# Optimization experiments

Hardware: AMD Instinct MI355X
Metric: run time of the kernel (lower is better)

The kernel has to match this reference:

```python
import jax, jax.numpy as jnp
import numpy as np

K = 2                 # top-k experts per token
CAP_FACTOR = 1.25     # capacity factor


def setup_inputs() -> dict:
    key = jax.random.key(0)
    ks = jax.random.split(key, 6)
    B, T, C, H, E = 8, 2048, 1024, 4096, 8
    return {
        "x":  jax.random.normal(ks[0], (B, T, C), dtype=jnp.float32),
        "Wr": jax.random.normal(ks[1], (C, E), dtype=jnp.float32) * 0.02,
        "W1": jax.random.normal(ks[2], (E, C, H), dtype=jnp.float32) * 0.02,
        "b1": jax.random.normal(ks[3], (E, H), dtype=jnp.float32) * 0.02,
        "W2": jax.random.normal(ks[4], (E, H, C), dtype=jnp.float32) * 0.02,
        "b2": jax.random.normal(ks[5], (E, C), dtype=jnp.float32) * 0.02,
    }


def reference(x, Wr, W1, b1, W2, b2):
    B, T, C = x.shape
    E = Wr.shape[1]
    capacity = int(T / E * CAP_FACTOR)  # per (expert, batch-row) bucket, as in torch code

    # Router: probs over experts, top-k selection
    probs = jax.nn.softmax(x @ Wr, axis=-1)                  # [B,T,E]
    topk_probs, topk_experts = jax.lax.top_k(probs, K)       # [B,T,K]

    # Flatten token slots in (t, k) order -- matches torch nonzero() enumeration
    S = T * K
    e_flat = topk_experts.reshape(B, S)                      # [B,S] int32
    p_flat = topk_probs.reshape(B, S)                        # [B,S]
    x_rep = jnp.repeat(x, K, axis=1)                         # [B,S,C]; slot (t,k) -> x[b,t]

    # Position of each slot within its (batch-row b, expert e) group
    onehot = jax.nn.one_hot(e_flat, E, dtype=jnp.int32)      # [B,S,E]
    pos_all = jnp.cumsum(onehot, axis=1) - onehot            # position before self
    pos = jnp.take_along_axis(pos_all, e_flat[..., None], axis=-1)[..., 0]  # [B,S]
    keep = pos < capacity                                    # tokens beyond capacity dropped
    pos_c = jnp.minimum(pos, capacity - 1)

    # Dispatch: scatter kept tokens into [E, B, capacity, C] buffer (padding_val = 0)
    b_idx = jnp.broadcast_to(jnp.arange(B)[:, None], (B, S))
    buf = jnp.zeros((E, B, capacity, C), dtype=x.dtype)
    buf = buf.at[e_flat, b_idx, pos_c].add(x_rep * keep[..., None].astype(x.dtype))

    # Expert FFN (grouped GEMM): Linear -> ReLU -> Linear, one weight set per expert
    h = jax.nn.relu(jnp.einsum('ebnc,ech->ebnh', buf, W1) + b1[:, None, None, :])
    y = jnp.einsum('ebnh,ehc->ebnc', h, W2) + b2[:, None, None, :]

    # Combine: gather back, zero dropped slots, weight by router prob, sum over k
    y_tok = y[e_flat, b_idx, pos_c]                          # [B,S,C]
    y_tok = y_tok * (keep[..., None].astype(x.dtype)) * p_flat[..., None]
    out = y_tok.reshape(B, T, K, C).sum(axis=2)              # [B,T,C]
    return out
```

## Files before the change

### kernel.cpp

```cpp
#include <hip/hip_runtime.h>

#define B_ 8
#define T_ 2048
#define C_ 1024
#define H_ 4096
#define E_ 8
#define S_ (2 * T_)
#define CAP 320
#define ME 2560
#define NROWS (E_ * ME)

typedef __attribute__((ext_vector_type(8))) short short8;
typedef __attribute__((ext_vector_type(4))) float f32x4;

__device__ __forceinline__ unsigned short f2bf(float f) {
  unsigned u = __float_as_uint(f);
  unsigned r = 0x7FFFu + ((u >> 16) & 1u);
  return (unsigned short)((u + r) >> 16);
}
__device__ __forceinline__ float bf2f(unsigned short u) {
  return __uint_as_float(((unsigned)u) << 16);
}

__device__ __forceinline__ void gload_lds16(const void* g, void* l) {
  __builtin_amdgcn_global_load_lds(
      (const __attribute__((address_space(1))) unsigned int*)g,
      (__attribute__((address_space(3))) unsigned int*)l, 16, 0, 0);
}

__global__ void cvt_transpose(const float* __restrict__ in,
                              unsigned short* __restrict__ out, int R, int Cc) {
  __shared__ float t[64][65];
  const int tid = threadIdx.x;
  const long eoff = (long)blockIdx.z * R * Cc;
  const int r0 = blockIdx.x * 64, c0 = blockIdx.y * 64;
#pragma unroll
  for (int it = 0; it < 4; ++it) {
    int r = it * 16 + (tid >> 4);
    int c = (tid & 15) * 4;
    float4 v = *(const float4*)(in + eoff + (long)(r0 + r) * Cc + c0 + c);
    t[r][c] = v.x; t[r][c + 1] = v.y; t[r][c + 2] = v.z; t[r][c + 3] = v.w;
  }
  __syncthreads();
#pragma unroll
  for (int it = 0; it < 4; ++it) {
    int oc = it * 16 + (tid >> 4);
    int orr = (tid & 15) * 4;
    union { unsigned short u[4]; unsigned long long ll; } o;
    o.u[0] = f2bf(t[orr + 0][oc]); o.u[1] = f2bf(t[orr + 1][oc]);
    o.u[2] = f2bf(t[orr + 2][oc]); o.u[3] = f2bf(t[orr + 3][oc]);
    *(unsigned long long*)(out + eoff + (long)(c0 + oc) * R + r0 + orr) = o.ll;
  }
}

__global__ void router_cvt(const float* __restrict__ x, const float* __restrict__ Wr,
                           int* __restrict__ es, float* __restrict__ ps,
                           unsigned short* __restrict__ x_bf) {
  const int token = blockIdx.x * 4 + (threadIdx.x >> 6);
  const int lane = threadIdx.x & 63;
  const float* xr = x + (long)token * C_;
  float acc[8] = {0, 0, 0, 0, 0, 0, 0, 0};
#pragma unroll
  for (int j = 0; j < 4; ++j) {
    int c = j * 256 + lane * 4;
    float4 xv = *(const float4*)(xr + c);
    union { unsigned short u[4]; unsigned long long ll; } o;
    o.u[0] = f2bf(xv.x); o.u[1] = f2bf(xv.y); o.u[2] = f2bf(xv.z); o.u[3] = f2bf(xv.w);
    *(unsigned long long*)(x_bf + (long)token * C_ + c) = o.ll;
    const float xe[4] = {xv.x, xv.y, xv.z, xv.w};
#pragma unroll
    for (int i = 0; i < 4; ++i) {
      const float4* wr = (const float4*)(Wr + (long)(c + i) * 8);
      float4 w0 = wr[0], w1 = wr[1];
      float v = xe[i];
      acc[0] += v * w0.x; acc[1] += v * w0.y; acc[2] += v * w0.z; acc[3] += v * w0.w;
      acc[4] += v * w1.x; acc[5] += v * w1.y; acc[6] += v * w1.z; acc[7] += v * w1.w;
    }
  }
#pragma unroll
  for (int off = 32; off >= 1; off >>= 1)
#pragma unroll
    for (int e = 0; e < 8; ++e) acc[e] += __shfl_xor(acc[e], off);
  float mx = acc[0];
#pragma unroll
  for (int e = 1; e < 8; ++e) mx = fmaxf(mx, acc[e]);
  float pr[8], se = 0.f;
#pragma unroll
  for (int e = 0; e < 8; ++e) { pr[e] = expf(acc[e] - mx); se += pr[e]; }
  float inv = 1.f / se;
  int e0 = 0; float v0 = pr[0];
#pragma unroll
  for (int e = 1; e < 8; ++e) if (pr[e] > v0) { v0 = pr[e]; e0 = e; }
  int e1 = -1; float v1 = -1.f;
#pragma unroll
  for (int e = 0; e < 8; ++e) if (e != e0 && pr[e] > v1) { v1 = pr[e]; e1 = e; }
  if (lane == 0) {
    es[2 * token] = e0;     ps[2 * token] = v0 * inv;
    es[2 * token + 1] = e1; ps[2 * token + 1] = v1 * inv;
  }
}

__global__ void positions(const int* __restrict__ es, int* __restrict__ pos,
                          int* __restrict__ tsrc) {
  const int b = blockIdx.x;
  const int lane = threadIdx.x;
  int cnt[8] = {0, 0, 0, 0, 0, 0, 0, 0};
  unsigned long long below = (1ULL << lane) - 1ULL;
  int e_next = es[(long)b * S_ + lane];
  for (int chunk = 0; chunk < S_ / 64; ++chunk) {
    int e = e_next;
    if (chunk + 1 < S_ / 64) e_next = es[(long)b * S_ + (chunk + 1) * 64 + lane];
    int myPos = 0;
#pragma unroll
    for (int ei = 0; ei < 8; ++ei) {
      unsigned long long m = __ballot(e == ei);
      if (e == ei) myPos = cnt[ei] + __popcll(m & below);
      cnt[ei] += __popcll(m);
    }
    int s = chunk * 64 + lane;
    pos[(long)b * S_ + s] = myPos;
    if (myPos < CAP)
      tsrc[(long)e * ME + b * CAP + myPos] = b * T_ + (s >> 1);
  }
}

template <bool GATHER, bool RELU>
__global__ __launch_bounds__(512, 2) void moe_gemm256(
    const unsigned short* __restrict__ A, const unsigned short* __restrict__ BT,
    const float* __restrict__ bias, const int* __restrict__ tsrc,
    unsigned short* __restrict__ outp, const int Kfull, const int Kslice,
    const int NT, const int KS) {
  constexpr int BK = 64;
  constexpr int MT = ME / 256;
  __shared__ unsigned short As[2][256 * BK];
  __shared__ unsigned short Bs[2][256 * BK];
  const int tid = threadIdx.x, lane = tid & 63, w = tid >> 6;
  const int wr = w >> 2, wc = w & 3;
  const int N = NT * 256;

  const int nwg = E_ * KS * NT * MT;
  const int chunk = nwg >> 3;
  const int swz = (blockIdx.x & 7) * chunk + (blockIdx.x >> 3);
  const int mt = swz % MT;
  int rem = swz / MT;
  const int nt = rem % NT; rem /= NT;
  const int ks = rem % KS;
  const int e = rem / KS;
  const int n0 = nt * 256;
  const long ksoff = (long)ks * Kslice;

  const unsigned short* aPtr[4];
#pragma unroll
  for (int hh = 0; hh < 2; ++hh)
#pragma unroll
    for (int i = 0; i < 2; ++i) {
      int r = hh * 128 + i * 64 + w * 8 + (lane >> 3);
      int p = lane & 7;
      long rowbase;
      if constexpr (GATHER) {
        int xrow = tsrc[(long)e * ME + mt * 256 + r];
        if (xrow < 0) xrow = 0;
        rowbase = (long)xrow * Kfull;
      } else {
        rowbase = ((long)e * ME + mt * 256 + r) * (long)Kfull;
      }
      aPtr[hh * 2 + i] = A + rowbase + ksoff + ((p ^ (r & 7)) << 3);
    }
  const unsigned short* bPtr[4];
#pragma unroll
  for (int hh = 0; hh < 2; ++hh)
#pragma unroll
    for (int i = 0; i < 2; ++i) {
      int r = hh * 128 + i * 64 + w * 8 + (lane >> 3);
      int p = lane & 7;
      bPtr[hh * 2 + i] =
          BT + ((long)e * N + n0 + r) * (long)Kfull + ksoff + ((p ^ (r & 7)) << 3);
    }

  f32x4 acc[8][4];
#pragma unroll
  for (int m = 0; m < 8; ++m)
#pragma unroll
    for (int n = 0; n < 4; ++n) acc[m][n] = (f32x4){0.f, 0.f, 0.f, 0.f};

  const int l15 = lane & 15, l4 = lane >> 4;

#pragma unroll
  for (int hh = 0; hh < 2; ++hh)
#pragma unroll
    for (int i = 0; i < 2; ++i) {
      gload_lds16(aPtr[hh * 2 + i], &As[0][(hh * 128 + i * 64 + w * 8) * BK]);
      gload_lds16(bPtr[hh * 2 + i], &Bs[0][(hh * 128 + i * 64 + w * 8) * BK]);
    }
  __syncthreads();

  const int nkt = Kslice / BK;
  int cur = 0;
  for (int kt = 0; kt < nkt; ++kt) {
    const bool pf = (kt + 1 < nkt);
    const long koff = (long)(kt + 1) * BK;
    short8 bfr[4][2];
#pragma unroll
    for (int q = 0; q < 4; ++q) {
      if (q == 0) {
#pragma unroll
        for (int n = 0; n < 4; ++n)
#pragma unroll
          for (int s = 0; s < 2; ++s) {
            int r = wc * 64 + n * 16 + l15;
            int slot = (s * 4 + l4) ^ (r & 7);
            bfr[n][s] = *(const short8*)&Bs[cur][r * BK + slot * 8];
          }
      }
      short8 af[2][2];
#pragma unroll
      for (int mi = 0; mi < 2; ++mi)
#pragma unroll
        for (int s = 0; s < 2; ++s) {
          int r = wr * 128 + (q * 2 + mi) * 16 + l15;
          int slot = (s * 4 + l4) ^ (r & 7);
          af[mi][s] = *(const short8*)&As[cur][r * BK + slot * 8];
        }
      if (pf) {
        if (q < 2) {
          gload_lds16(aPtr[q * 2 + 0] + koff,
                      &As[cur ^ 1][(q * 128 + 0 + w * 8) * BK]);
          gload_lds16(aPtr[q * 2 + 1] + koff,
                      &As[cur ^ 1][(q * 128 + 64 + w * 8) * BK]);
        } else {
          gload_lds16(bPtr[(q - 2) * 2 + 0] + koff,
                      &Bs[cur ^ 1][((q - 2) * 128 + 0 + w * 8) * BK]);
          gload_lds16(bPtr[(q - 2) * 2 + 1] + koff,
                      &Bs[cur ^ 1][((q - 2) * 128 + 64 + w * 8) * BK]);
        }
      }
      asm volatile("s_waitcnt lgkmcnt(0)" ::: "memory");
      __builtin_amdgcn_sched_barrier(0);
      __builtin_amdgcn_s_setprio(1);
#pragma unroll
      for (int mi = 0; mi < 2; ++mi)
#pragma unroll
        for (int n = 0; n < 4; ++n)
#pragma unroll
          for (int s = 0; s < 2; ++s)
            acc[q * 2 + mi][n] = __builtin_amdgcn_mfma_f32_16x16x32_bf16(
                af[mi][s], bfr[n][s], acc[q * 2 + mi][n], 0, 0, 0);
      __builtin_amdgcn_s_setprio(0);
      __builtin_amdgcn_sched_barrier(0);
    }
    __syncthreads();
    cur ^= 1;
  }

  const long rbase = (long)ks * NROWS + (long)e * ME + mt * 256;
#pragma unroll
  for (int m = 0; m < 8; ++m) {
#pragma unroll
    for (int n = 0; n < 4; ++n) {
      const int trow = wr * 128 + m * 16 + (l4 << 2);
      const int col = n0 + wc * 64 + n * 16 + l15;
      const float bv = (ks == 0) ? bias[(long)e * N + col] : 0.f;
#pragma unroll
      for (int j = 0; j < 4; ++j) {
        float v = acc[m][n][j] + bv;
        if constexpr (RELU) v = fmaxf(v, 0.f);
        outp[(rbase + trow + j) * (long)N + col] = f2bf(v);
      }
    }
  }
}

__global__ void combine(const unsigned short* __restrict__ y,
                        const int* __restrict__ es, const float* __restrict__ ps,
                        const int* __restrict__ pos, float* __restrict__ out) {
  const int token = blockIdx.x;
  const int b = token >> 11;
  const int s0 = 2 * token, s1 = s0 + 1;
  int e0 = es[s0], e1 = es[s1];
  int q0 = pos[s0], q1 = pos[s1];
  float p0 = ps[s0], p1 = ps[s1];
  const bool k0 = q0 < CAP, k1 = q1 < CAP;
  if (q0 > CAP - 1) q0 = CAP - 1;
  if (q1 > CAP - 1) q1 = CAP - 1;
  const long half = (long)NROWS * C_;
  const unsigned short* r0 = y + ((long)e0 * ME + b * CAP + q0) * C_;
  const unsigned short* r1 = y + ((long)e1 * ME + b * CAP + q1) * C_;
  const int c = threadIdx.x * 4;
  float4 a = {0.f, 0.f, 0.f, 0.f};
  if (k0) {
    union { unsigned short u[4]; unsigned long long ll; } v, vv;
    v.ll = *(const unsigned long long*)(r0 + c);
    vv.ll = *(const unsigned long long*)(r0 + half + c);
    a.x += p0 * (bf2f(v.u[0]) + bf2f(vv.u[0]));
    a.y += p0 * (bf2f(v.u[1]) + bf2f(vv.u[1]));
    a.z += p0 * (bf2f(v.u[2]) + bf2f(vv.u[2]));
    a.w += p0 * (bf2f(v.u[3]) + bf2f(vv.u[3]));
  }
  if (k1) {
    union { unsigned short u[4]; unsigned long long ll; } v, vv;
    v.ll = *(const unsigned long long*)(r1 + c);
    vv.ll = *(const unsigned long long*)(r1 + half + c);
    a.x += p1 * (bf2f(v.u[0]) + bf2f(vv.u[0]));
    a.y += p1 * (bf2f(v.u[1]) + bf2f(vv.u[1]));
    a.z += p1 * (bf2f(v.u[2]) + bf2f(vv.u[2]));
    a.w += p1 * (bf2f(v.u[3]) + bf2f(vv.u[3]));
  }
  *(float4*)(out + (long)token * C_ + c) = a;
}

extern "C" void kernel_launch(void* const* d_in, const int* in_sizes, int n_in,
                              void* d_out, int out_size, void* d_ws, size_t ws_size,
                              hipStream_t stream) {
  const float* x = (const float*)d_in[0];
  const float* Wr = (const float*)d_in[1];
  const float* W1 = (const float*)d_in[2];
  const float* b1 = (const float*)d_in[3];
  const float* W2 = (const float*)d_in[4];
  const float* b2 = (const float*)d_in[5];
  float* out = (float*)d_out;
  char* ws = (char*)d_ws;
  unsigned short* x_bf = (unsigned short*)(ws + 0L);
  unsigned short* W1T = (unsigned short*)(ws + 33554432L);
  unsigned short* W2T = (unsigned short*)(ws + 100663296L);
  unsigned short* h = (unsigned short*)(ws + 167772160L);
  unsigned short* y = (unsigned short*)(ws + 335544320L);
  int* es = (int*)(ws + 419430400L);
  float* ps = (float*)(ws + 419561472L);
  int* pos = (int*)(ws + 419692544L);
  int* tsrc = (int*)(ws + 419823616L);

  cvt_transpose<<<dim3(16, 64, 8), 256, 0, stream>>>(W1, W1T, C_, H_);
  cvt_transpose<<<dim3(64, 16, 8), 256, 0, stream>>>(W2, W2T, H_, C_);
  router_cvt<<<4096, 256, 0, stream>>>(x, Wr, es, ps, x_bf);
  hipMemsetAsync(tsrc, 0xFF, NROWS * sizeof(int), stream);
  positions<<<8, 64, 0, stream>>>(es, pos, tsrc);
  moe_gemm256<true, true><<<1280, 512, 0, stream>>>(x_bf, W1T, b1, tsrc, h,
                                                    C_, C_, 16, 1);
  moe_gemm256<false, false><<<640, 512, 0, stream>>>(h, W2T, b2, nullptr, y,
                                                     H_, H_ / 2, 4, 2);
  combine<<<16384, 256, 0, stream>>>(y, es, ps, pos, out);
}
```

Before: 578.2 us.

## Split K-tile LDS into two half-slices with fine-grained vmcnt waits

Restructures the GEMM main loop so each 64-wide K tile is stored as two 32-wide LDS sub-buffers with a new XOR swizzle. Each half is loaded and consumed separately, and partial s_waitcnt vmcnt counts plus raw s_barrier replace the full __syncthreads. The aim is to overlap global-to-LDS prefetch with MFMA at finer granularity and cut barrier stalls. The risk is synchronisation correctness: the sub-buffers of the next stage may be overwritten while other waves still read them, and the vmcnt accounting must match the number of loads issued.

New measurement: 596.8 us. 3.2% more time.

```diff
diff --git a/kernel.cpp b/kernel.cpp
--- a/kernel.cpp
+++ b/kernel.cpp
@@ -132,8 +132,8 @@
     const int NT, const int KS) {
   constexpr int BK = 64;
   constexpr int MT = ME / 256;
-  __shared__ unsigned short As[2][256 * BK];
-  __shared__ unsigned short Bs[2][256 * BK];
+  __shared__ unsigned short As[2][2][256 * 32];
+  __shared__ unsigned short Bs[2][2][256 * 32];
   const int tid = threadIdx.x, lane = tid & 63, w = tid >> 6;
   const int wr = w >> 2, wc = w & 3;
   const int N = NT * 256;
@@ -149,33 +149,25 @@
   const int n0 = nt * 256;
   const long ksoff = (long)ks * Kslice;
 
-  const unsigned short* aPtr[4];
-#pragma unroll
-  for (int hh = 0; hh < 2; ++hh)
-#pragma unroll
-    for (int i = 0; i < 2; ++i) {
-      int r = hh * 128 + i * 64 + w * 8 + (lane >> 3);
-      int p = lane & 7;
-      long rowbase;
-      if constexpr (GATHER) {
-        int xrow = tsrc[(long)e * ME + mt * 256 + r];
-        if (xrow < 0) xrow = 0;
-        rowbase = (long)xrow * Kfull;
-      } else {
-        rowbase = ((long)e * ME + mt * 256 + r) * (long)Kfull;
-      }
-      aPtr[hh * 2 + i] = A + rowbase + ksoff + ((p ^ (r & 7)) << 3);
-    }
-  const unsigned short* bPtr[4];
-#pragma unroll
-  for (int hh = 0; hh < 2; ++hh)
-#pragma unroll
-    for (int i = 0; i < 2; ++i) {
-      int r = hh * 128 + i * 64 + w * 8 + (lane >> 3);
-      int p = lane & 7;
-      bPtr[hh * 2 + i] =
-          BT + ((long)e * N + n0 + r) * (long)Kfull + ksoff + ((p ^ (r & 7)) << 3);
-    }
+  const int srow = lane >> 2;
+  const int psrc = ((lane & 3) ^ ((lane >> 3) & 3)) << 3;
+  const unsigned short* aSrc[2];
+  const unsigned short* bSrc[2];
+#pragma unroll
+  for (int i = 0; i < 2; ++i) {
+    int r = i * 128 + w * 16 + srow;
+    long rowbase;
+    if constexpr (GATHER) {
+      int xrow = tsrc[(long)e * ME + mt * 256 + r];
+      if (xrow < 0) xrow = 0;
+      rowbase = (long)xrow * Kfull;
+    } else {
+      rowbase = ((long)e * ME + mt * 256 + r) * (long)Kfull;
+    }
+    aSrc[i] = A + rowbase + ksoff + psrc;
+    bSrc[i] = BT + ((long)e * N + n0 + i * 128 + w * 16 + srow) * (long)Kfull +
+              ksoff + psrc;
+  }
 
   f32x4 acc[8][4];
 #pragma unroll
@@ -184,73 +176,68 @@
     for (int n = 0; n < 4; ++n) acc[m][n] = (f32x4){0.f, 0.f, 0.f, 0.f};
 
   const int l15 = lane & 15, l4 = lane >> 4;
-
-#pragma unroll
-  for (int hh = 0; hh < 2; ++hh)
-#pragma unroll
-    for (int i = 0; i < 2; ++i) {
-      gload_lds16(aPtr[hh * 2 + i], &As[0][(hh * 128 + i * 64 + w * 8) * BK]);
-      gload_lds16(bPtr[hh * 2 + i], &Bs[0][(hh * 128 + i * 64 + w * 8) * BK]);
-    }
-  __syncthreads();
+  const int rslot = ((l4 ^ ((l15 >> 1) & 3)) << 3);
+
+#pragma unroll
+  for (int s = 0; s < 2; ++s) {
+#pragma unroll
+    for (int i = 0; i < 2; ++i)
+      gload_lds16(aSrc[i] + s * 32, &As[0][s][(i * 128 + w * 16) * 32]);
+#pragma unroll
+    for (int i = 0; i < 2; ++i)
+      gload_lds16(bSrc[i] + s * 32, &Bs[0][s][(i * 128 + w * 16) * 32]);
+  }
+  asm volatile("s_waitcnt vmcnt(4)" ::: "memory");
+  __builtin_amdgcn_s_barrier();
+  __builtin_amdgcn_sched_barrier(0);
 
   const int nkt = Kslice / BK;
-  int cur = 0;
   for (int kt = 0; kt < nkt; ++kt) {
+    const int cur = kt & 1, nxt = cur ^ 1;
     const bool pf = (kt + 1 < nkt);
     const long koff = (long)(kt + 1) * BK;
-    short8 bfr[4][2];
-#pragma unroll
-    for (int q = 0; q < 4; ++q) {
-      if (q == 0) {
+#pragma unroll
+    for (int s = 0; s < 2; ++s) {
+      short8 bf[4], af[8];
+#pragma unroll
+      for (int n = 0; n < 4; ++n) {
+        int rb = wc * 64 + n * 16 + l15;
+        bf[n] = *(const short8*)&Bs[cur][s][rb * 32 + rslot];
+      }
+#pragma unroll
+      for (int m = 0; m < 8; ++m) {
+        int r = wr * 128 + m * 16 + l15;
+        af[m] = *(const short8*)&As[cur][s][r * 32 + rslot];
+      }
+      if (pf) {
+#pragma unroll
+        for (int i = 0; i < 2; ++i)
+          gload_lds16(aSrc[i] + koff + s * 32, &As[nxt][s][(i * 128 + w * 16) * 32]);
+#pragma unroll
+        for (int i = 0; i < 2; ++i)
+          gload_lds16(bSrc[i] + koff + s * 32, &Bs[nxt][s][(i * 128 + w * 16) * 32]);
+      }
+      __builtin_amdgcn_s_setprio(1);
+#pragma unroll
+      for (int m = 0; m < 8; ++m)
 #pragma unroll
         for (int n = 0; n < 4; ++n)
-#pragma unroll
-          for (int s = 0; s < 2; ++s) {
-            int r = wc * 64 + n * 16 + l15;
-            int slot = (s * 4 + l4) ^ (r & 7);
-            bfr[n][s] = *(const short8*)&Bs[cur][r * BK + slot * 8];
-          }
-      }
-      short8 af[2][2];
-#pragma unroll
-      for (int mi = 0; mi < 2; ++mi)
-#pragma unroll
-        for (int s = 0; s < 2; ++s) {
-          int r = wr * 128 + (q * 2 + mi) * 16 + l15;
-          int slot = (s * 4 + l4) ^ (r & 7);
-          af[mi][s] = *(const short8*)&As[cur][r * BK + slot * 8];
-        }
-      if (pf) {
-        if (q < 2) {
-          gload_lds16(aPtr[q * 2 + 0] + koff,
-                      &As[cur ^ 1][(q * 128 + 0 + w * 8) * BK]);
-          gload_lds16(aPtr[q * 2 + 1] + koff,
-                      &As[cur ^ 1][(q * 128 + 64 + w * 8) * BK]);
-        } else {
-          gload_lds16(bPtr[(q - 2) * 2 + 0] + koff,
-                      &Bs[cur ^ 1][((q - 2) * 128 + 0 + w * 8) * BK]);
-          gload_lds16(bPtr[(q - 2) * 2 + 1] + koff,
-                      &Bs[cur ^ 1][((q - 2) * 128 + 64 + w * 8) * BK]);
-        }
-      }
-      asm volatile("s_waitcnt lgkmcnt(0)" ::: "memory");
-      __builtin_amdgcn_sched_barrier(0);
-      __builtin_amdgcn_s_setprio(1);
-#pragma unroll
-      for (int mi = 0; mi < 2; ++mi)
-#pragma unroll
-        for (int n = 0; n < 4; ++n)
-#pragma unroll
-          for (int s = 0; s < 2; ++s)
-            acc[q * 2 + mi][n] = __builtin_amdgcn_mfma_f32_16x16x32_bf16(
-                af[mi][s], bfr[n][s], acc[q * 2 + mi][n], 0, 0, 0);
+          acc[m][n] = __builtin_amdgcn_mfma_f32_16x16x32_bf16(af[m], bf[n],
+                                                              acc[m][n], 0, 0, 0);
       __builtin_amdgcn_s_setprio(0);
       __builtin_amdgcn_sched_barrier(0);
-    }
-    __syncthreads();
-    cur ^= 1;
-  }
+      if (s == 0) {
+        if (pf) asm volatile("s_waitcnt vmcnt(4)" ::: "memory");
+        else    asm volatile("s_waitcnt vmcnt(0)" ::: "memory");
+        __builtin_amdgcn_s_barrier();
+      } else if (pf) {
+        asm volatile("s_waitcnt vmcnt(4)" ::: "memory");
+        __builtin_amdgcn_s_barrier();
+      }
+      __builtin_amdgcn_sched_barrier(0);
+    }
+  }
+  __builtin_amdgcn_sched_barrier(0);
 
   const long rbase = (long)ks * NROWS + (long)e * ME + mt * 256;
 #pragma unroll
```
